# Optimization experiments

Hardware: AMD Instinct MI355X
Metric: run time of the kernel (lower is better)

Reference implementation:

```python
import jax, jax.numpy as jnp
import numpy as np

N, D, E, OUT = 50000, 256, 320000, 1

def setup_inputs() -> dict:
    key = jax.random.key(0)
    k1, k2, k3, k4, k5, k6 = jax.random.split(key, 6)
    z = jax.random.normal(k1, (N, D), dtype=jnp.float32)
    edge_index = jax.random.randint(k2, (2, E), 0, N, dtype=jnp.int64)
    # xavier_normal for fc1: std = sqrt(2/(fan_in+fan_out)) = sqrt(2/(2D+D))
    w1 = jax.random.normal(k3, (D, 2 * D), dtype=jnp.float32) * np.sqrt(2.0 / (3 * D))
    b1 = jnp.zeros((D,), dtype=jnp.float32)
    w2 = jax.random.normal(k4, (OUT, D), dtype=jnp.float32) * np.sqrt(2.0 / (D + OUT))
    b2 = jnp.zeros((OUT,), dtype=jnp.float32)
    return {"z": z, "edge_index": edge_index, "w1": w1, "b1": b1, "w2": w2, "b2": b2}

def reference(z, edge_index, w1, b1, w2, b2):
    x1 = z[edge_index[0]]                     # [E, D]
    x2 = z[edge_index[1]]                     # [E, D]
    x = jnp.concatenate([x1, x2], axis=1)     # [E, 2D]
    h = jax.nn.relu(x @ w1.T + b1)            # [E, D]
    return h @ w2.T + b2                      # [E, OUT]
```

## Files before the change

### kernel.cpp

```cpp
#include <hip/hip_runtime.h>
#include <hip/hip_bf16.h>

#define D 256
#define TWOD 512
#define BM 128
#define BK 32

typedef __attribute__((ext_vector_type(8))) __bf16 bf16x8;
typedef __attribute__((ext_vector_type(4))) float f32x4;
typedef __attribute__((ext_vector_type(8))) unsigned short ushort8;

using as1_u32 = __attribute__((address_space(1))) const unsigned int;
using as3_u32 = __attribute__((address_space(3))) unsigned int;

__device__ __forceinline__ void gload_lds16(const void* g, void* l) {
    __builtin_amdgcn_global_load_lds((as1_u32*)g, (as3_u32*)l, 16, 0, 0);
}

__device__ __forceinline__ float bf2f(unsigned short u) {
    unsigned int x = ((unsigned int)u) << 16;
    return __uint_as_float(x);
}
__device__ __forceinline__ unsigned short f2bf_bits(float f) {
    unsigned int x = __float_as_uint(f);
    unsigned int r = (x + 0x7fffu + ((x >> 16) & 1u)) >> 16;
    return (unsigned short)r;
}

__global__ __launch_bounds__(256) void wt_conv_kernel(
    const float* __restrict__ w1, unsigned short* __restrict__ WtP)
{
    const int s = blockIdx.x * 256 + threadIdx.x;
    const int o = s >> 9;
    const int i = s & 511;
    const float v = w1[s];
    const int jj = (i < D) ? o : (D + o);
    const int k  = (i < D) ? i : (i - D);
    const int c16 = jj >> 4, r = jj & 15;
    const int kblk = k >> 5, kin = k & 31;
    const int g = kin >> 3, kj = kin & 7;
    WtP[(size_t)((c16 * 8 + kblk) * 512 + (r + 16 * g) * 8 + kj)] = f2bf_bits(v);
}

__global__ __launch_bounds__(256, 3) void node_proj_mfma(
    const float* __restrict__ z, const unsigned short* __restrict__ WtP,
    unsigned short* __restrict__ C, int M, int Mblocks)
{
    __shared__ __align__(16) float Abuf[3][BM * BK];

    const int bid    = blockIdx.x;
    const int rowblk = (bid >> 5) * 8 + (bid & 7);
    if (rowblk >= Mblocks) return;
    const int m0 = rowblk * BM;
    const int cb = ((bid >> 3) & 3) * BM;

    const int t    = threadIdx.x;
    const int lane = t & 63;
    const int w    = t >> 6;

    const int r16 = lane & 15;
    const int g   = lane >> 4;

    const int wm = (w >> 1) * 64;
    const int wn = (w & 1) * 64;
    const int c16b = (cb + wn) >> 4;

    f32x4 acc[4][4];
    #pragma unroll
    for (int mt = 0; mt < 4; ++mt)
        #pragma unroll
        for (int nt = 0; nt < 4; ++nt)
            acc[mt][nt] = (f32x4){0.f, 0.f, 0.f, 0.f};

    auto stageA = [&](int buf, int k0) {
        #pragma unroll
        for (int i = 0; i < 4; ++i) {
            const int c = i * 256 + t;
            const int r = c >> 3;
            const int q = c & 7;
            const int col = ((q ^ (r & 7)) << 2);
            const int row = min(m0 + r, M - 1);
            const float* gsrc = z + (size_t)row * D + k0 + col;
            float* ldst = &Abuf[buf][(size_t)(i * 256 + w * 64) * 4];
            gload_lds16(gsrc, ldst);
        }
    };

    bf16x8 bb[2][4];
    auto loadB = [&](int par, int kt) {
        #pragma unroll
        for (int nt = 0; nt < 4; ++nt) {
            const ushort8 bu = *(const ushort8*)(
                WtP + (size_t)(((c16b + nt) * 8 + kt) * 512 + lane * 8));
            bb[par][nt] = __builtin_bit_cast(bf16x8, bu);
        }
    };

    stageA(0, 0);
    stageA(1, BK);
    __builtin_amdgcn_sched_barrier(0);
    loadB(0, 0);

    #pragma unroll
    for (int kt = 0; kt < 8; ++kt) {
        if (kt == 0 || kt == 7) asm volatile("s_waitcnt vmcnt(8)" ::: "memory");
        else                    asm volatile("s_waitcnt vmcnt(12)" ::: "memory");
        __builtin_amdgcn_s_barrier();

        if (kt < 6) stageA((kt + 2) % 3, (kt + 2) * BK);
        __builtin_amdgcn_sched_barrier(0);
        if (kt < 7) loadB((kt + 1) & 1, kt + 1);

        bf16x8 a[4];
        #pragma unroll
        for (int mt = 0; mt < 4; ++mt) {
            const int rl = wm + mt * 16 + r16;
            const int sw = rl & 7;
            const f32x4 f0 = *(const f32x4*)&Abuf[kt % 3][rl * 32 + (((2 * g) ^ sw) << 2)];
            const f32x4 f1 = *(const f32x4*)&Abuf[kt % 3][rl * 32 + (((2 * g + 1) ^ sw) << 2)];
            bf16x8 tt;
            tt[0] = (__bf16)f0[0]; tt[1] = (__bf16)f0[1];
            tt[2] = (__bf16)f0[2]; tt[3] = (__bf16)f0[3];
            tt[4] = (__bf16)f1[0]; tt[5] = (__bf16)f1[1];
            tt[6] = (__bf16)f1[2]; tt[7] = (__bf16)f1[3];
            a[mt] = tt;
        }

        __builtin_amdgcn_s_setprio(1);
        #pragma unroll
        for (int nt = 0; nt < 4; ++nt)
            #pragma unroll
            for (int mt = 0; mt < 4; ++mt)
                acc[mt][nt] = __builtin_amdgcn_mfma_f32_16x16x32_bf16(
                    bb[kt & 1][nt], a[mt], acc[mt][nt], 0, 0, 0);
        __builtin_amdgcn_s_setprio(0);
    }

    #pragma unroll
    for (int mt = 0; mt < 4; ++mt) {
        const int row = m0 + wm + mt * 16 + r16;
        if (row < M) {
            #pragma unroll
            for (int nt = 0; nt < 4; ++nt) {
                const int col = cb + wn + nt * 16 + g * 4;
                ushort4 pk;
                pk.x = f2bf_bits(acc[mt][nt][0]);
                pk.y = f2bf_bits(acc[mt][nt][1]);
                pk.z = f2bf_bits(acc[mt][nt][2]);
                pk.w = f2bf_bits(acc[mt][nt][3]);
                *(ushort4*)(C + (size_t)row * TWOD + col) = pk;
            }
        }
    }
}

__global__ __launch_bounds__(256) void edge_kernel(
    const int* __restrict__ ei, const unsigned short* __restrict__ C,
    const float* __restrict__ b1, const float* __restrict__ w2,
    const float* __restrict__ b2, float* __restrict__ out, int E)
{
    const int h   = threadIdx.x & 31;
    const int gid = (blockIdx.x * blockDim.x + threadIdx.x) >> 5;
    const int ng  = (gridDim.x * blockDim.x) >> 5;
    const int j0  = h * 8;

    const float4 w2a = *(const float4*)(w2 + j0);
    const float4 w2b = *(const float4*)(w2 + j0 + 4);
    const float4 b1a = *(const float4*)(b1 + j0);
    const float4 b1b = *(const float4*)(b1 + j0 + 4);
    const float  b2s = b2[0];

    auto dot8 = [&](const ushort8& ua, const ushort8& ub) -> float {
        float s;
        s  = fmaxf(bf2f(ua[0]) + bf2f(ub[0]) + b1a.x, 0.f) * w2a.x;
        s += fmaxf(bf2f(ua[1]) + bf2f(ub[1]) + b1a.y, 0.f) * w2a.y;
        s += fmaxf(bf2f(ua[2]) + bf2f(ub[2]) + b1a.z, 0.f) * w2a.z;
        s += fmaxf(bf2f(ua[3]) + bf2f(ub[3]) + b1a.w, 0.f) * w2a.w;
        s += fmaxf(bf2f(ua[4]) + bf2f(ub[4]) + b1b.x, 0.f) * w2b.x;
        s += fmaxf(bf2f(ua[5]) + bf2f(ub[5]) + b1b.y, 0.f) * w2b.y;
        s += fmaxf(bf2f(ua[6]) + bf2f(ub[6]) + b1b.z, 0.f) * w2b.z;
        s += fmaxf(bf2f(ua[7]) + bf2f(ub[7]) + b1b.w, 0.f) * w2b.w;
        return s;
    };

    int e = gid;
    for (; e + 3 * ng < E; e += 4 * ng) {
        const int e1 = e + ng, e2 = e + 2 * ng, e3 = e + 3 * ng;
        const int u0 = ei[e],  v0 = ei[E + e];
        const int u1 = ei[e1], v1 = ei[E + e1];
        const int u2 = ei[e2], v2 = ei[E + e2];
        const int u3 = ei[e3], v3 = ei[E + e3];

        const ushort8 ua0 = *(const ushort8*)(C + (size_t)u0 * TWOD + j0);
        const ushort8 ub0 = *(const ushort8*)(C + (size_t)v0 * TWOD + D + j0);
        const ushort8 ua1 = *(const ushort8*)(C + (size_t)u1 * TWOD + j0);
        const ushort8 ub1 = *(const ushort8*)(C + (size_t)v1 * TWOD + D + j0);
        const ushort8 ua2 = *(const ushort8*)(C + (size_t)u2 * TWOD + j0);
        const ushort8 ub2 = *(const ushort8*)(C + (size_t)v2 * TWOD + D + j0);
        const ushort8 ua3 = *(const ushort8*)(C + (size_t)u3 * TWOD + j0);
        const ushort8 ub3 = *(const ushort8*)(C + (size_t)v3 * TWOD + D + j0);

        float s0 = dot8(ua0, ub0);
        float s1 = dot8(ua1, ub1);
        float s2 = dot8(ua2, ub2);
        float s3 = dot8(ua3, ub3);

        #pragma unroll
        for (int off = 16; off; off >>= 1) {
            s0 += __shfl_xor(s0, off);
            s1 += __shfl_xor(s1, off);
            s2 += __shfl_xor(s2, off);
            s3 += __shfl_xor(s3, off);
        }

        if (h == 0) {
            out[e]  = s0 + b2s;
            out[e1] = s1 + b2s;
            out[e2] = s2 + b2s;
            out[e3] = s3 + b2s;
        }
    }
    for (; e < E; e += ng) {
        const int u = ei[e], v = ei[E + e];
        const ushort8 ua = *(const ushort8*)(C + (size_t)u * TWOD + j0);
        const ushort8 ub = *(const ushort8*)(C + (size_t)v * TWOD + D + j0);
        float s = dot8(ua, ub);
        #pragma unroll
        for (int off = 16; off; off >>= 1)
            s += __shfl_xor(s, off);
        if (h == 0) out[e] = s + b2s;
    }
}

extern "C" void kernel_launch(void* const* d_in, const int* in_sizes, int n_in,
                              void* d_out, int out_size, void* d_ws, size_t ws_size,
                              hipStream_t stream) {
    const float* z  = (const float*)d_in[0];
    const int*   ei = (const int*)d_in[1];
    const float* w1 = (const float*)d_in[2];
    const float* b1 = (const float*)d_in[3];
    const float* w2 = (const float*)d_in[4];
    const float* b2 = (const float*)d_in[5];
    float* out = (float*)d_out;

    const int M = in_sizes[0] / D;
    const int E = in_sizes[1] / 2;

    unsigned short* C   = (unsigned short*)d_ws;
    unsigned short* WtP = (unsigned short*)d_out;

    wt_conv_kernel<<<512, 256, 0, stream>>>(w1, WtP);

    const int Mblocks = (M + BM - 1) / BM;
    const int stripes = (Mblocks + 7) / 8;
    node_proj_mfma<<<stripes * 32, 256, 0, stream>>>(z, WtP, C, M, Mblocks);

    edge_kernel<<<4096, 256, 0, stream>>>(ei, C, b1, w2, b2, out, E);
}
```

Baseline: 88.03 us.

## Fold b1 into node projection and batch eight edges per half-wave gather

Adds the fc1 bias into the first half of the projected node table at GEMM epilogue time, so the edge kernel no longer adds b1 per edge. The edge kernel drops the grid-stride loop: each 32-lane group now handles eight consecutive edges, issuing all index loads and then all sixteen row gathers before computing, which puts more memory requests in flight. It launches one block per 64 edges instead of a fixed 4096-block grid. Register pressure rises with eight ushort8 pairs per lane, and the bias is now rounded to bf16 together with the projection.

```diff
diff --git a/kernel.cpp b/kernel.cpp
--- a/kernel.cpp
+++ b/kernel.cpp
@@ -44,7 +44,8 @@
 
 __global__ __launch_bounds__(256, 3) void node_proj_mfma(
     const float* __restrict__ z, const unsigned short* __restrict__ WtP,
-    unsigned short* __restrict__ C, int M, int Mblocks)
+    const float* __restrict__ b1, unsigned short* __restrict__ C,
+    int M, int Mblocks)
 {
     __shared__ __align__(16) float Abuf[3][BM * BK];
 
@@ -143,11 +144,16 @@
             #pragma unroll
             for (int nt = 0; nt < 4; ++nt) {
                 const int col = cb + wn + nt * 16 + g * 4;
+                f32x4 av = acc[mt][nt];
+                if (col < D) {
+                    const float4 bv = *(const float4*)(b1 + col);
+                    av[0] += bv.x; av[1] += bv.y; av[2] += bv.z; av[3] += bv.w;
+                }
                 ushort4 pk;
-                pk.x = f2bf_bits(acc[mt][nt][0]);
-                pk.y = f2bf_bits(acc[mt][nt][1]);
-                pk.z = f2bf_bits(acc[mt][nt][2]);
-                pk.w = f2bf_bits(acc[mt][nt][3]);
+                pk.x = f2bf_bits(av[0]);
+                pk.y = f2bf_bits(av[1]);
+                pk.z = f2bf_bits(av[2]);
+                pk.w = f2bf_bits(av[3]);
                 *(ushort4*)(C + (size_t)row * TWOD + col) = pk;
             }
         }
@@ -156,79 +162,60 @@
 
 __global__ __launch_bounds__(256) void edge_kernel(
     const int* __restrict__ ei, const unsigned short* __restrict__ C,
-    const float* __restrict__ b1, const float* __restrict__ w2,
-    const float* __restrict__ b2, float* __restrict__ out, int E)
+    const float* __restrict__ w2, const float* __restrict__ b2,
+    float* __restrict__ out, int E)
 {
     const int h   = threadIdx.x & 31;
     const int gid = (blockIdx.x * blockDim.x + threadIdx.x) >> 5;
-    const int ng  = (gridDim.x * blockDim.x) >> 5;
     const int j0  = h * 8;
+    const int e0  = gid * 8;
+    if (e0 >= E) return;
 
     const float4 w2a = *(const float4*)(w2 + j0);
     const float4 w2b = *(const float4*)(w2 + j0 + 4);
-    const float4 b1a = *(const float4*)(b1 + j0);
-    const float4 b1b = *(const float4*)(b1 + j0 + 4);
     const float  b2s = b2[0];
 
-    auto dot8 = [&](const ushort8& ua, const ushort8& ub) -> float {
-        float s;
-        s  = fmaxf(bf2f(ua[0]) + bf2f(ub[0]) + b1a.x, 0.f) * w2a.x;
-        s += fmaxf(bf2f(ua[1]) + bf2f(ub[1]) + b1a.y, 0.f) * w2a.y;
-        s += fmaxf(bf2f(ua[2]) + bf2f(ub[2]) + b1a.z, 0.f) * w2a.z;
-        s += fmaxf(bf2f(ua[3]) + bf2f(ub[3]) + b1a.w, 0.f) * w2a.w;
-        s += fmaxf(bf2f(ua[4]) + bf2f(ub[4]) + b1b.x, 0.f) * w2b.x;
-        s += fmaxf(bf2f(ua[5]) + bf2f(ub[5]) + b1b.y, 0.f) * w2b.y;
-        s += fmaxf(bf2f(ua[6]) + bf2f(ub[6]) + b1b.z, 0.f) * w2b.z;
-        s += fmaxf(bf2f(ua[7]) + bf2f(ub[7]) + b1b.w, 0.f) * w2b.w;
-        return s;
-    };
-
-    int e = gid;
-    for (; e + 3 * ng < E; e += 4 * ng) {
-        const int e1 = e + ng, e2 = e + 2 * ng, e3 = e + 3 * ng;
-        const int u0 = ei[e],  v0 = ei[E + e];
-        const int u1 = ei[e1], v1 = ei[E + e1];
-        const int u2 = ei[e2], v2 = ei[E + e2];
-        const int u3 = ei[e3], v3 = ei[E + e3];
-
-        const ushort8 ua0 = *(const ushort8*)(C + (size_t)u0 * TWOD + j0);
-        const ushort8 ub0 = *(const ushort8*)(C + (size_t)v0 * TWOD + D + j0);
-        const ushort8 ua1 = *(const ushort8*)(C + (size_t)u1 * TWOD + j0);
-        const ushort8 ub1 = *(const ushort8*)(C + (size_t)v1 * TWOD + D + j0);
-        const ushort8 ua2 = *(const ushort8*)(C + (size_t)u2 * TWOD + j0);
-        const ushort8 ub2 = *(const ushort8*)(C + (size_t)v2 * TWOD + D + j0);
-        const ushort8 ua3 = *(const ushort8*)(C + (size_t)u3 * TWOD + j0);
-        const ushort8 ub3 = *(const ushort8*)(C + (size_t)v3 * TWOD + D + j0);
-
-        float s0 = dot8(ua0, ub0);
-        float s1 = dot8(ua1, ub1);
-        float s2 = dot8(ua2, ub2);
-        float s3 = dot8(ua3, ub3);
-
-        #pragma unroll
-        for (int off = 16; off; off >>= 1) {
-            s0 += __shfl_xor(s0, off);
-            s1 += __shfl_xor(s1, off);
-            s2 += __shfl_xor(s2, off);
-            s3 += __shfl_xor(s3, off);
-        }
-
-        if (h == 0) {
-            out[e]  = s0 + b2s;
-            out[e1] = s1 + b2s;
-            out[e2] = s2 + b2s;
-            out[e3] = s3 + b2s;
-        }
-    }
-    for (; e < E; e += ng) {
-        const int u = ei[e], v = ei[E + e];
-        const ushort8 ua = *(const ushort8*)(C + (size_t)u * TWOD + j0);
-        const ushort8 ub = *(const ushort8*)(C + (size_t)v * TWOD + D + j0);
-        float s = dot8(ua, ub);
-        #pragma unroll
-        for (int off = 16; off; off >>= 1)
-            s += __shfl_xor(s, off);
-        if (h == 0) out[e] = s + b2s;
+    int u[8], v[8];
+    #pragma unroll
+    for (int i = 0; i < 8; ++i) {
+        const int e = min(e0 + i, E - 1);
+        u[i] = ei[e];
+        v[i] = ei[E + e];
+    }
+
+    ushort8 ua[8], ub[8];
+    #pragma unroll
+    for (int i = 0; i < 8; ++i) {
+        ua[i] = *(const ushort8*)(C + (size_t)u[i] * TWOD + j0);
+        ub[i] = *(const ushort8*)(C + (size_t)v[i] * TWOD + D + j0);
+    }
+
+    float s[8];
+    #pragma unroll
+    for (int i = 0; i < 8; ++i) {
+        float acc = 0.f;
+        acc += fmaxf(bf2f(ua[i][0]) + bf2f(ub[i][0]), 0.f) * w2a.x;
+        acc += fmaxf(bf2f(ua[i][1]) + bf2f(ub[i][1]), 0.f) * w2a.y;
+        acc += fmaxf(bf2f(ua[i][2]) + bf2f(ub[i][2]), 0.f) * w2a.z;
+        acc += fmaxf(bf2f(ua[i][3]) + bf2f(ub[i][3]), 0.f) * w2a.w;
+        acc += fmaxf(bf2f(ua[i][4]) + bf2f(ub[i][4]), 0.f) * w2b.x;
+        acc += fmaxf(bf2f(ua[i][5]) + bf2f(ub[i][5]), 0.f) * w2b.y;
+        acc += fmaxf(bf2f(ua[i][6]) + bf2f(ub[i][6]), 0.f) * w2b.z;
+        acc += fmaxf(bf2f(ua[i][7]) + bf2f(ub[i][7]), 0.f) * w2b.w;
+        s[i] = acc;
+    }
+
+    #pragma unroll
+    for (int off = 16; off; off >>= 1) {
+        #pragma unroll
+        for (int i = 0; i < 8; ++i)
+            s[i] += __shfl_xor(s[i], off);
+    }
+
+    if (h == 0) {
+        #pragma unroll
+        for (int i = 0; i < 8; ++i)
+            if (e0 + i < E) out[e0 + i] = s[i] + b2s;
     }
 }
 
@@ -253,7 +240,8 @@
 
     const int Mblocks = (M + BM - 1) / BM;
     const int stripes = (Mblocks + 7) / 8;
-    node_proj_mfma<<<stripes * 32, 256, 0, stream>>>(z, WtP, C, M, Mblocks);
-
-    edge_kernel<<<4096, 256, 0, stream>>>(ei, C, b1, w2, b2, out, E);
-}
+    node_proj_mfma<<<stripes * 32, 256, 0, stream>>>(z, WtP, b1, C, M, Mblocks);
+
+    const int hw = (E + 7) / 8;
+    edge_kernel<<<(hw + 7) / 8, 256, 0, stream>>>(ei, C, w2, b2, out, E);
+}
```

After: 90.20 us. +2.5%, slower.
